# Performance work log

Measured on AMD Instinct MI355X. Metric: run time of the kernel, lower is better.

## Reference

```python
import jax, jax.numpy as jnp
import numpy as np

B, T, D = 32, 512, 768
K, H = 256, 512


def setup_inputs() -> dict:
    key = jax.random.key(0)
    ks = jax.random.split(key, 5)
    s = 0.02  # keep pre-activations in a sane range
    return {
        "inputs": jax.random.normal(ks[0], (B, T, D), jnp.float32),
        "W_x": jax.random.normal(ks[1], (K + 1, 4 * H), jnp.float32) * s,
        "W_h": jax.random.normal(ks[2], (H, 4 * H), jnp.float32) * s,
        "b_lstm": jnp.zeros((4 * H,), jnp.float32),
        "W_key": jax.random.normal(ks[3], (H, K), jnp.float32) * s,
        "b_key": jnp.zeros((K,), jnp.float32),
        "W_g": jax.random.normal(ks[4], (H, 1), jnp.float32) * s,
        "b_g": jnp.zeros((1,), jnp.float32),
        "conf_gain": jnp.ones((), jnp.float32),
        "conf_bias": jnp.zeros((), jnp.float32),
    }


def reference(inputs, W_x, W_h, b_lstm, W_key, b_key, W_g, b_g, conf_gain, conf_bias):
    Bq, Tq, Dq = inputs.shape
    Kq = W_key.shape[1]
    Hq = W_h.shape[0]
    t_idx = jnp.arange(Tq)
    xs = jnp.transpose(inputs, (1, 0, 2))  # [T, B, D]

    def step(carry, xt):
        t, x = xt  # t: scalar step index, x: [B, D]
        key_r, h, c, M_k, M_v = carry
        # Keras LSTMCell (gate order i, f, c, o); input is previous key_r [B, K+1]
        z = key_r @ W_x + h @ W_h + b_lstm
        i, f, g_c, o = jnp.split(z, 4, axis=-1)
        i = jax.nn.sigmoid(i)
        f = jax.nn.sigmoid(f)
        g_c = jnp.tanh(g_c)
        o = jax.nn.sigmoid(o)
        c = f * c + i * g_c
        h = o * jnp.tanh(c)  # lstm_out == hidden in Keras LSTMCell
        key_w = h @ W_key + b_key            # [B, K]
        g = jax.nn.sigmoid(h @ W_g + b_g)    # [B, 1]
        # similarity attention over all previously written memory slots
        sim = jnp.einsum('bd,tbd->bt', x, M_v)          # [B, T]
        mask = (t_idx < t)[None, :]                     # valid slots only
        w_k = jax.nn.softmax(jnp.where(mask, sim, -1e30), axis=1)
        c_k = jax.nn.sigmoid(sim * conf_gain + conf_bias)
        aug = jnp.concatenate([jnp.transpose(M_k, (1, 0, 2)), c_k[:, :, None]], axis=2)  # [B, T, K+1]
        key_r_new = jnp.where(t > 0, g * jnp.einsum('bt,btk->bk', w_k, aug), 0.0)
        M_k = M_k.at[t].set(key_w)
        M_v = M_v.at[t].set(x)
        return (key_r_new, h, c, M_k, M_v), None

    init = (
        jnp.zeros((Bq, Kq + 1), inputs.dtype),
        jnp.zeros((Bq, Hq), inputs.dtype),
        jnp.zeros((Bq, Hq), inputs.dtype),
        jnp.zeros((Tq, Bq, Kq), inputs.dtype),
        jnp.zeros((Tq, Bq, Dq), inputs.dtype),
    )
    (key_r, h, c, M_k, M_v), _ = jax.lax.scan(step, init, (t_idx, xs))
    return h  # final lstm_out
```

## Files before the change

### kernel.cpp

```cpp
#include <hip/hip_runtime.h>
#include <math.h>

#define BQ 32
#define TQ 512
#define DQ 768
#define KQ 256
#define HQ 512
#define G4 2048
#define SROW 772
#define NWG 512
#define NTHR 256
#define NBG 4

typedef float f32x4 __attribute__((ext_vector_type(4)));

__device__ __forceinline__ void waitcnt0() {
  asm volatile("s_waitcnt vmcnt(0) lgkmcnt(0)" ::: "memory");
}
__device__ __forceinline__ void st_agent(float* p, float v) {
  asm volatile("global_store_dword %0, %1, off sc0 sc1" :: "v"(p), "v"(v) : "memory");
}
__device__ __forceinline__ int ld_flag(const int* p) {
  int v;
  asm volatile("global_load_dword %0, %1, off sc0 sc1\ns_waitcnt vmcnt(0)"
               : "=v"(v) : "v"(p) : "memory");
  return v;
}
__device__ __forceinline__ void wg_wait(const int* flags, int target) {
  const int lane = threadIdx.x & 63;
  for (;;) {
    int v = ld_flag(flags + lane);
    if (__all(v >= target)) break;
    __builtin_amdgcn_s_sleep(1);
  }
  __syncthreads();
}
__device__ __forceinline__ void wg_signal(int* flag, int val) {
  waitcnt0();
  __syncthreads();
  if (threadIdx.x == 0)
    asm volatile("global_store_dword %0, %1, off sc0 sc1" :: "v"(flag), "v"(val) : "memory");
}
__device__ __forceinline__ float sigm(float x) { return 1.f / (1.f + __expf(-x)); }

__global__ void __launch_bounds__(256) gram_k(const float* __restrict__ X,
                                              float* __restrict__ Gm) {
  __shared__ __align__(16) float As[64 * 33];
  __shared__ __align__(16) float Bs[64 * 33];
  const int bid = blockIdx.x;
  const int b = blockIdx.y;
  int I = 0, base = 0;
  while (base + I + 1 <= bid) { base += I + 1; ++I; }
  const int J = bid - base;
  const int t0 = I * 64, u0 = J * 64;
  const float* Xb = X + (size_t)b * TQ * DQ;
  const int ty = threadIdx.x >> 4, tx = threadIdx.x & 15;
  const int sc = threadIdx.x & 31, sr = threadIdx.x >> 5;
  float acc[4][4];
#pragma unroll
  for (int i = 0; i < 4; ++i)
#pragma unroll
    for (int j = 0; j < 4; ++j) acc[i][j] = 0.f;
  for (int k0 = 0; k0 < DQ; k0 += 32) {
#pragma unroll
    for (int rr = 0; rr < 8; ++rr) {
      const int r = rr * 8 + sr;
      As[r * 33 + sc] = Xb[(size_t)(t0 + r) * DQ + k0 + sc];
      Bs[r * 33 + sc] = Xb[(size_t)(u0 + r) * DQ + k0 + sc];
    }
    __syncthreads();
#pragma unroll
    for (int k = 0; k < 32; ++k) {
      float av[4], bv[4];
#pragma unroll
      for (int i = 0; i < 4; ++i) av[i] = As[(ty * 4 + i) * 33 + k];
#pragma unroll
      for (int j = 0; j < 4; ++j) bv[j] = Bs[(tx * 4 + j) * 33 + k];
#pragma unroll
      for (int i = 0; i < 4; ++i)
#pragma unroll
        for (int j = 0; j < 4; ++j) acc[i][j] += av[i] * bv[j];
    }
    __syncthreads();
  }
  float* gb = Gm + (size_t)b * TQ * TQ;
#pragma unroll
  for (int i = 0; i < 4; ++i) {
    f32x4 o;
    o.x = acc[i][0]; o.y = acc[i][1]; o.z = acc[i][2]; o.w = acc[i][3];
    *(f32x4*)&gb[(size_t)(t0 + ty * 4 + i) * TQ + u0 + tx * 4] = o;
  }
}

__global__ void __launch_bounds__(256) smax_k(float* __restrict__ Gm,
                                              float* __restrict__ Sv,
                                              const float* __restrict__ cgp,
                                              const float* __restrict__ cbp) {
  const int t = blockIdx.x + 1;
  const int b = blockIdx.y;
  const int tid = threadIdx.x;
  const int lane = tid & 63;
  const int wv = tid >> 6;
  __shared__ float row[TQ];
  __shared__ float r1[4], r2[4], r3[4];
  float* R = Gm + ((size_t)b * TQ + t) * TQ;
  const float cg = cgp[0], cb = cbp[0];
  for (int i = tid; i < t; i += 256) row[i] = R[i];
  __syncthreads();
  float m = -3e38f;
  for (int i = tid; i < t; i += 256) m = fmaxf(m, row[i]);
#pragma unroll
  for (int k = 1; k < 64; k <<= 1) m = fmaxf(m, __shfl_xor(m, k));
  if (lane == 0) r1[wv] = m;
  __syncthreads();
  m = fmaxf(fmaxf(r1[0], r1[1]), fmaxf(r1[2], r1[3]));
  float s = 0.f, sck = 0.f;
  for (int i = tid; i < t; i += 256) {
    const float r = row[i];
    const float e = __expf(r - m);
    const float ck = 1.f / (1.f + __expf(-(r * cg + cb)));
    row[i] = e; s += e; sck += e * ck;
  }
#pragma unroll
  for (int k = 1; k < 64; k <<= 1) { s += __shfl_xor(s, k); sck += __shfl_xor(sck, k); }
  if (lane == 0) { r2[wv] = s; r3[wv] = sck; }
  __syncthreads();
  s = r2[0] + r2[1] + r2[2] + r2[3];
  sck = r3[0] + r3[1] + r3[2] + r3[3];
  const float inv = 1.f / s;
  for (int i = tid; i < t; i += 256) R[i] = row[i] * inv;
  if (tid == 0) Sv[(size_t)b * TQ + t] = sck * inv;
}

__global__ void __launch_bounds__(NTHR, 2) esbn_scan(
    const float* __restrict__ Wx, const float* __restrict__ Wh,
    const float* __restrict__ bl, const float* __restrict__ Wk,
    const float* __restrict__ bk, const float* __restrict__ Wg,
    const float* __restrict__ bgp, const float* __restrict__ Wmat,
    const float* __restrict__ Sv, float* buf, int* flagsX, int* flagsY,
    float* __restrict__ out) {
  __shared__ __align__(16) float st[NBG * SROW];
  __shared__ __align__(16) float wrow[NBG * TQ];
  __shared__ __align__(16) float Mk_s[16 * 520];
  __shared__ __align__(16) float wkey_s[4 * 520];
  __shared__ float wgv[HQ];
  __shared__ __align__(16) float zred[4 * 8 * 4 * 4];
  __shared__ float c_s[NBG * 8];
  __shared__ float gg_s[NBG];
  __shared__ float A_s[NBG * 4];
  __shared__ float bl_s[32];
  __shared__ float bk_s[4];
  __shared__ float bg_s;

  const int tid = threadIdx.x;
  const int wg = blockIdx.x & 63;
  const int grp = blockIdx.x >> 6;
  const int b0 = grp * NBG;
  const int dc = tid >> 3;
  const int cg = tid & 7;

  int colg[4];
#pragma unroll
  for (int j = 0; j < 4; ++j) {
    const int c = cg * 4 + j;
    colg[j] = (c >> 3) * HQ + wg * 8 + (c & 7);
  }
  f32x4 wh[16], wxr[8], wxl;
#pragma unroll
  for (int i = 0; i < 16; ++i) {
    const int d = (i << 5) + dc;
    wh[i].x = Wh[(size_t)d * G4 + colg[0]];
    wh[i].y = Wh[(size_t)d * G4 + colg[1]];
    wh[i].z = Wh[(size_t)d * G4 + colg[2]];
    wh[i].w = Wh[(size_t)d * G4 + colg[3]];
  }
#pragma unroll
  for (int i = 0; i < 8; ++i) {
    const int d = (i << 5) + dc;
    wxr[i].x = Wx[(size_t)d * G4 + colg[0]];
    wxr[i].y = Wx[(size_t)d * G4 + colg[1]];
    wxr[i].z = Wx[(size_t)d * G4 + colg[2]];
    wxr[i].w = Wx[(size_t)d * G4 + colg[3]];
  }
  wxl.x = wxl.y = wxl.z = wxl.w = 0.f;
  if (dc == 0) {
    wxl.x = Wx[(size_t)256 * G4 + colg[0]];
    wxl.y = Wx[(size_t)256 * G4 + colg[1]];
    wxl.z = Wx[(size_t)256 * G4 + colg[2]];
    wxl.w = Wx[(size_t)256 * G4 + colg[3]];
  }
  for (int i = tid; i < NBG * SROW; i += NTHR) st[i] = 0.f;
  for (int i = tid; i < 16 * 520; i += NTHR) Mk_s[i] = 0.f;
  for (int i = tid; i < 4 * 520; i += NTHR) {
    const int kl = i / 520, u = i - kl * 520;
    wkey_s[i] = (u < HQ) ? Wk[(size_t)u * KQ + wg * 4 + kl] : 0.f;
  }
  for (int i = tid; i < HQ; i += NTHR) wgv[i] = Wg[i];
  if (tid < 32) bl_s[tid] = bl[(tid >> 3) * HQ + wg * 8 + (tid & 7)];
  if (tid < 4) bk_s[tid] = bk[wg * 4 + tid];
  if (tid == 0) bg_s = bgp[0];
  if (tid < NBG * 8) c_s[tid] = 0.f;
  if (tid < NBG * 4) A_s[tid] = 0.f;
  __syncthreads();

  int* fx = flagsX + grp * 64;
  int* fy = flagsY + grp * 64;
  const int yb = tid >> 6;
  const int ykl = (tid >> 4) & 3;
  const int ytc = tid & 15;
  const int lt = tid & 63;

  for (int t = 0; t < TQ; ++t) {
    const int p = t & 1, pn = p ^ 1;
    f32x4 acc[NBG];
#pragma unroll
    for (int b = 0; b < NBG; ++b) { acc[b].x = 0.f; acc[b].y = 0.f; acc[b].z = 0.f; acc[b].w = 0.f; }
#pragma unroll
    for (int i = 0; i < 16; ++i) {
      const f32x4 w = wh[i];
      const int d = (i << 5) + dc;
#pragma unroll
      for (int b = 0; b < NBG; ++b) acc[b] += st[b * SROW + d] * w;
    }
    wg_wait(fy, t);
    {
      float* base = buf + (size_t)(p * BQ + b0) * SROW;
      const int r0 = tid / 65, o0 = tid - r0 * 65;
      const float* q0 = base + r0 * SROW + 512 + (o0 << 2);
      f32x4 u0, u1;
      u1.x = u1.y = u1.z = u1.w = 0.f;
      asm volatile("global_load_dwordx4 %0, %1, off sc0 sc1" : "=v"(u0) : "v"(q0));
      if (tid < 4) {
        const int j1 = tid + 256;
        const int r1 = j1 / 65, o1 = j1 - r1 * 65;
        const float* q1 = base + r1 * SROW + 512 + (o1 << 2);
        asm volatile("global_load_dwordx4 %0, %1, off sc0 sc1" : "=v"(u1) : "v"(q1));
      }
      asm volatile("s_waitcnt vmcnt(0)" : "+v"(u0), "+v"(u1) : : "memory");
      *(f32x4*)&st[r0 * SROW + 512 + (o0 << 2)] = u0;
      if (tid < 4) {
        const int j1 = tid + 256;
        const int r1 = j1 / 65, o1 = j1 - r1 * 65;
        *(f32x4*)&st[r1 * SROW + 512 + (o1 << 2)] = u1;
      }
    }
    __syncthreads();
#pragma unroll
    for (int i = 0; i < 8; ++i) {
      const f32x4 w = wxr[i];
      const int d = 512 + (i << 5) + dc;
#pragma unroll
      for (int b = 0; b < NBG; ++b) acc[b] += st[b * SROW + d] * w;
    }
    if (dc == 0) {
#pragma unroll
      for (int b = 0; b < NBG; ++b) acc[b] += st[b * SROW + 768] * wxl;
    }
#pragma unroll
    for (int m = 8; m <= 32; m <<= 1) {
#pragma unroll
      for (int b = 0; b < NBG; ++b) {
        acc[b].x += __shfl_xor(acc[b].x, m);
        acc[b].y += __shfl_xor(acc[b].y, m);
        acc[b].z += __shfl_xor(acc[b].z, m);
        acc[b].w += __shfl_xor(acc[b].w, m);
      }
    }
    if (lt < 8) {
      const int wv = tid >> 6;
#pragma unroll
      for (int b = 0; b < NBG; ++b)
        *(f32x4*)&zred[((wv * 8 + lt) * 4 + b) * 4] = acc[b];
    }
    __syncthreads();
    if (tid < 32) {
      const int b = tid >> 3, u = tid & 7;
      float zg[4];
#pragma unroll
      for (int g = 0; g < 4; ++g) {
        const int cgi = g * 2 + (u >> 2), comp = u & 3;
        float z = bl_s[g * 8 + u];
#pragma unroll
        for (int wv = 0; wv < 4; ++wv) z += zred[((wv * 8 + cgi) * 4 + b) * 4 + comp];
        zg[g] = z;
      }
      const float gi = sigm(zg[0]);
      const float gf = sigm(zg[1]);
      const float go = sigm(zg[3]);
      const float cn = gf * c_s[tid] + gi * tanhf(zg[2]);
      const float hv = go * tanhf(cn);
      c_s[tid] = cn;
      st_agent(buf + (size_t)(pn * BQ + b0 + b) * SROW + wg * 8 + u, hv);
      if (t == TQ - 1) out[(size_t)(b0 + b) * HQ + wg * 8 + u] = hv;
    }
    wg_signal(&fx[wg], t + 1);
    if (t == TQ - 1) break;

    if (t > 0) {
      const float* wr = Wmat + ((size_t)(b0 + yb) * TQ + t) * TQ;
#pragma unroll
      for (int k = 0; k < 8; ++k) {
        const int u = lt + (k << 6);
        wrow[yb * TQ + u] = (u < t) ? wr[u] : 0.f;
      }
    }
    __syncthreads();
    float accA = 0.f;
    if (t > 0) {
      const float* mk = &Mk_s[(yb * 4 + ykl) * 520];
      const float* wb = &wrow[yb * TQ];
#pragma unroll
      for (int j = 0; j < 32; ++j) {
        const int u = ytc + (j << 4);
        accA += wb[u] * mk[u];
      }
      accA += __shfl_xor(accA, 1);
      accA += __shfl_xor(accA, 2);
      accA += __shfl_xor(accA, 4);
      accA += __shfl_xor(accA, 8);
    }
    if (ytc == 0) A_s[yb * 4 + ykl] = accA;
    wg_wait(fx, t + 1);
    {
      float* base = buf + (size_t)(pn * BQ + b0) * SROW;
      f32x4 v0, v1;
      const int i0 = tid, i1 = tid + 256;
      const float* p0 = base + (i0 >> 7) * SROW + ((i0 & 127) << 2);
      const float* p1v = base + (i1 >> 7) * SROW + ((i1 & 127) << 2);
      asm volatile("global_load_dwordx4 %0, %1, off sc0 sc1" : "=v"(v0) : "v"(p0));
      asm volatile("global_load_dwordx4 %0, %1, off sc0 sc1" : "=v"(v1) : "v"(p1v));
      asm volatile("s_waitcnt vmcnt(0)" : "+v"(v0), "+v"(v1) : : "memory");
      *(f32x4*)&st[(i0 >> 7) * SROW + ((i0 & 127) << 2)] = v0;
      *(f32x4*)&st[(i1 >> 7) * SROW + ((i1 & 127) << 2)] = v1;
    }
    __syncthreads();
    {
      float a = 0.f;
#pragma unroll
      for (int k = 0; k < 8; ++k) {
        const int u = lt + (k << 6);
        a += st[yb * SROW + u] * wgv[u];
      }
#pragma unroll
      for (int m = 1; m <= 32; m <<= 1) a += __shfl_xor(a, m);
      if (lt == 0) gg_s[yb] = sigm(a + bg_s);
    }
    __syncthreads();
    if (ytc == 0)
      st_agent(buf + (size_t)(pn * BQ + b0 + yb) * SROW + 512 + wg * 4 + ykl,
               gg_s[yb] * A_s[yb * 4 + ykl]);
    if (wg == 63 && lt == 0)
      st_agent(buf + (size_t)(pn * BQ + b0 + yb) * SROW + 512 + 256,
               gg_s[yb] * Sv[(size_t)(b0 + yb) * TQ + t]);
    wg_signal(&fy[wg], t + 1);
    {
      float kw = 0.f;
      const float* hrow = &st[yb * SROW];
      const float* wkr = &wkey_s[ykl * 520];
#pragma unroll
      for (int j = 0; j < 32; ++j) {
        const int u = ytc + (j << 4);
        kw += hrow[u] * wkr[u];
      }
      kw += __shfl_xor(kw, 1);
      kw += __shfl_xor(kw, 2);
      kw += __shfl_xor(kw, 4);
      kw += __shfl_xor(kw, 8);
      if (ytc == 0) Mk_s[(yb * 4 + ykl) * 520 + t] = kw + bk_s[ykl];
    }
  }
}

extern "C" void kernel_launch(void* const* d_in, const int* in_sizes, int n_in,
                              void* d_out, int out_size, void* d_ws, size_t ws_size,
                              hipStream_t stream) {
  (void)in_sizes; (void)n_in; (void)out_size; (void)ws_size;
  const float* X  = (const float*)d_in[0];
  const float* Wx = (const float*)d_in[1];
  const float* Wh = (const float*)d_in[2];
  const float* bl = (const float*)d_in[3];
  const float* Wk = (const float*)d_in[4];
  const float* bk = (const float*)d_in[5];
  const float* Wg = (const float*)d_in[6];
  const float* bg = (const float*)d_in[7];
  const float* cg = (const float*)d_in[8];
  const float* cb = (const float*)d_in[9];
  float* out = (float*)d_out;
  float* ws = (float*)d_ws;

  float* Gm = ws;
  float* Sv = ws + (size_t)8388608;
  float* buf = ws + (size_t)8404992;
  int* flagsX = (int*)(ws + (size_t)8454400);
  int* flagsY = flagsX + 512;

  hipMemsetAsync(Sv, 0, (size_t)(16384 + 49408 + 1024) * 4, stream);
  gram_k<<<dim3(36, BQ), dim3(256), 0, stream>>>(X, Gm);
  smax_k<<<dim3(TQ - 1, BQ), dim3(256), 0, stream>>>(Gm, Sv, cg, cb);

  void* args[] = {(void*)&Wx, (void*)&Wh, (void*)&bl, (void*)&Wk, (void*)&bk,
                  (void*)&Wg, (void*)&bg, (void*)&Gm, (void*)&Sv,
                  (void*)&buf, (void*)&flagsX, (void*)&flagsY, (void*)&out};
  hipError_t e = hipLaunchCooperativeKernel((const void*)esbn_scan, dim3(NWG),
                                            dim3(NTHR), args, 0, stream);
  if (e != hipSuccess) {
    esbn_scan<<<dim3(NWG), dim3(NTHR), 0, stream>>>(Wx, Wh, bl, Wk, bk, Wg, bg,
                                                    Gm, Sv, buf, flagsX,
                                                    flagsY, out);
  }
}
```

Baseline: 4.951 ms.

## Merge two per-step grid barriers into one by deferring gate scaling

Restructures the recurrent step so that each workgroup publishes its h slice and its unscaled attention readout together, then signals a single flag per step instead of two. The gate g is computed locally from h after the barrier and applied to the key_r contribution inside the z accumulation, rather than scaled before publication. The Wmat row loads are also prefetched early into registers. This removes one cross-workgroup barrier round trip per timestep, at the cost of each workgroup recomputing g and reading a larger combined buffer.

```diff
diff --git a/kernel.cpp b/kernel.cpp
--- a/kernel.cpp
+++ b/kernel.cpp
@@ -139,6 +139,7 @@
     const float* __restrict__ bgp, const float* __restrict__ Wmat,
     const float* __restrict__ Sv, float* buf, int* flagsX, int* flagsY,
     float* __restrict__ out) {
+  (void)flagsY;
   __shared__ __align__(16) float st[NBG * SROW];
   __shared__ __align__(16) float wrow[NBG * TQ];
   __shared__ __align__(16) float Mk_s[16 * 520];
@@ -147,7 +148,6 @@
   __shared__ __align__(16) float zred[4 * 8 * 4 * 4];
   __shared__ float c_s[NBG * 8];
   __shared__ float gg_s[NBG];
-  __shared__ float A_s[NBG * 4];
   __shared__ float bl_s[32];
   __shared__ float bk_s[4];
   __shared__ float bg_s;
@@ -200,21 +200,67 @@
   if (tid < 4) bk_s[tid] = bk[wg * 4 + tid];
   if (tid == 0) bg_s = bgp[0];
   if (tid < NBG * 8) c_s[tid] = 0.f;
-  if (tid < NBG * 4) A_s[tid] = 0.f;
-  __syncthreads();
-
-  int* fx = flagsX + grp * 64;
-  int* fy = flagsY + grp * 64;
+  __syncthreads();
+
+  int* f = flagsX + grp * 64;
   const int yb = tid >> 6;
   const int ykl = (tid >> 4) & 3;
   const int ytc = tid & 15;
   const int lt = tid & 63;
 
+  const int i0 = tid, i1 = tid + 256, i2 = tid + 512;
+  const int sb0 = i0 / 192, so0 = i0 - sb0 * 192;
+  const int sb1 = i1 / 192, so1 = i1 - sb1 * 192;
+  const int sb2 = i2 / 192, so2 = i2 - sb2 * 192;
+  const int sj0 = sb0 * SROW + ((so0 < 128) ? (so0 << 2) : (512 + ((so0 - 128) << 2)));
+  const int sj1 = sb1 * SROW + ((so1 < 128) ? (so1 << 2) : (512 + ((so1 - 128) << 2)));
+  const int sj2 = sb2 * SROW + ((so2 < 128) ? (so2 << 2) : (512 + ((so2 - 128) << 2)));
+
   for (int t = 0; t < TQ; ++t) {
     const int p = t & 1, pn = p ^ 1;
-    f32x4 acc[NBG];
-#pragma unroll
-    for (int b = 0; b < NBG; ++b) { acc[b].x = 0.f; acc[b].y = 0.f; acc[b].z = 0.f; acc[b].w = 0.f; }
+    float wv8[8];
+    const bool rowv = (t >= 1) && (t < TQ - 1);
+    if (rowv) {
+      const float* wr = Wmat + ((size_t)(b0 + yb) * TQ + t) * TQ + lt;
+#pragma unroll
+      for (int k = 0; k < 8; ++k) wv8[k] = wr[k << 6];
+    }
+    if (t > 0) {
+      wg_wait(f, t);
+      float* base = buf + (size_t)(p * BQ + b0) * SROW;
+      f32x4 v0, v1, v2;
+      const float* q0 = base + sj0;
+      const float* q1 = base + sj1;
+      const float* q2 = base + sj2;
+      asm volatile("global_load_dwordx4 %0, %1, off sc0 sc1" : "=v"(v0) : "v"(q0));
+      asm volatile("global_load_dwordx4 %0, %1, off sc0 sc1" : "=v"(v1) : "v"(q1));
+      asm volatile("global_load_dwordx4 %0, %1, off sc0 sc1" : "=v"(v2) : "v"(q2));
+      float sv = 0.f;
+      if (tid < 4) sv = Sv[(size_t)(b0 + tid) * TQ + (t - 1)];
+      asm volatile("s_waitcnt vmcnt(0)" : "+v"(v0), "+v"(v1), "+v"(v2) : : "memory");
+      *(f32x4*)&st[sj0] = v0;
+      *(f32x4*)&st[sj1] = v1;
+      *(f32x4*)&st[sj2] = v2;
+      if (tid < 4) st[tid * SROW + 768] = sv;
+    }
+    __syncthreads();
+    {
+      float a = 0.f;
+#pragma unroll
+      for (int k = 0; k < 8; ++k) {
+        const int u = lt + (k << 6);
+        a += st[yb * SROW + u] * wgv[u];
+      }
+#pragma unroll
+      for (int m = 1; m <= 32; m <<= 1) a += __shfl_xor(a, m);
+      if (lt == 0) gg_s[yb] = sigm(a + bg_s);
+    }
+    f32x4 acc[NBG], pk[NBG];
+#pragma unroll
+    for (int b = 0; b < NBG; ++b) {
+      acc[b].x = acc[b].y = acc[b].z = acc[b].w = 0.f;
+      pk[b].x = pk[b].y = pk[b].z = pk[b].w = 0.f;
+    }
 #pragma unroll
     for (int i = 0; i < 16; ++i) {
       const f32x4 w = wh[i];
@@ -222,39 +268,23 @@
 #pragma unroll
       for (int b = 0; b < NBG; ++b) acc[b] += st[b * SROW + d] * w;
     }
-    wg_wait(fy, t);
-    {
-      float* base = buf + (size_t)(p * BQ + b0) * SROW;
-      const int r0 = tid / 65, o0 = tid - r0 * 65;
-      const float* q0 = base + r0 * SROW + 512 + (o0 << 2);
-      f32x4 u0, u1;
-      u1.x = u1.y = u1.z = u1.w = 0.f;
-      asm volatile("global_load_dwordx4 %0, %1, off sc0 sc1" : "=v"(u0) : "v"(q0));
-      if (tid < 4) {
-        const int j1 = tid + 256;
-        const int r1 = j1 / 65, o1 = j1 - r1 * 65;
-        const float* q1 = base + r1 * SROW + 512 + (o1 << 2);
-        asm volatile("global_load_dwordx4 %0, %1, off sc0 sc1" : "=v"(u1) : "v"(q1));
-      }
-      asm volatile("s_waitcnt vmcnt(0)" : "+v"(u0), "+v"(u1) : : "memory");
-      *(f32x4*)&st[r0 * SROW + 512 + (o0 << 2)] = u0;
-      if (tid < 4) {
-        const int j1 = tid + 256;
-        const int r1 = j1 / 65, o1 = j1 - r1 * 65;
-        *(f32x4*)&st[r1 * SROW + 512 + (o1 << 2)] = u1;
-      }
-    }
-    __syncthreads();
 #pragma unroll
     for (int i = 0; i < 8; ++i) {
       const f32x4 w = wxr[i];
       const int d = 512 + (i << 5) + dc;
 #pragma unroll
-      for (int b = 0; b < NBG; ++b) acc[b] += st[b * SROW + d] * w;
+      for (int b = 0; b < NBG; ++b) pk[b] += st[b * SROW + d] * w;
     }
     if (dc == 0) {
 #pragma unroll
-      for (int b = 0; b < NBG; ++b) acc[b] += st[b * SROW + 768] * wxl;
+      for (int b = 0; b < NBG; ++b) pk[b] += st[b * SROW + 768] * wxl;
+    }
+    __syncthreads();
+#pragma unroll
+    for (int b = 0; b < NBG; ++b) {
+      const float g = gg_s[b];
+      acc[b].x += g * pk[b].x; acc[b].y += g * pk[b].y;
+      acc[b].z += g * pk[b].z; acc[b].w += g * pk[b].w;
     }
 #pragma unroll
     for (int m = 8; m <= 32; m <<= 1) {
@@ -290,23 +320,27 @@
       const float cn = gf * c_s[tid] + gi * tanhf(zg[2]);
       const float hv = go * tanhf(cn);
       c_s[tid] = cn;
-      st_agent(buf + (size_t)(pn * BQ + b0 + b) * SROW + wg * 8 + u, hv);
       if (t == TQ - 1) out[(size_t)(b0 + b) * HQ + wg * 8 + u] = hv;
-    }
-    wg_signal(&fx[wg], t + 1);
+      else st_agent(buf + (size_t)(pn * BQ + b0 + b) * SROW + wg * 8 + u, hv);
+    }
     if (t == TQ - 1) break;
-
-    if (t > 0) {
-      const float* wr = Wmat + ((size_t)(b0 + yb) * TQ + t) * TQ;
-#pragma unroll
-      for (int k = 0; k < 8; ++k) {
-        const int u = lt + (k << 6);
-        wrow[yb * TQ + u] = (u < t) ? wr[u] : 0.f;
-      }
-    }
-    __syncthreads();
-    float accA = 0.f;
-    if (t > 0) {
+    if (t >= 1) {
+#pragma unroll
+      for (int k = 0; k < 8; ++k) wrow[yb * TQ + lt + (k << 6)] = wv8[k];
+      float kw = 0.f;
+      const float* hrow = &st[yb * SROW];
+      const float* wkr = &wkey_s[ykl * 520];
+#pragma unroll
+      for (int j = 0; j < 32; ++j) {
+        const int u = ytc + (j << 4);
+        kw += hrow[u] * wkr[u];
+      }
+      kw += __shfl_xor(kw, 1);
+      kw += __shfl_xor(kw, 2);
+      kw += __shfl_xor(kw, 4);
+      kw += __shfl_xor(kw, 8);
+      if (ytc == 0) Mk_s[(yb * 4 + ykl) * 520 + (t - 1)] = kw + bk_s[ykl];
+      float accA = 0.f;
       const float* mk = &Mk_s[(yb * 4 + ykl) * 520];
       const float* wb = &wrow[yb * TQ];
 #pragma unroll
@@ -318,56 +352,10 @@
       accA += __shfl_xor(accA, 2);
       accA += __shfl_xor(accA, 4);
       accA += __shfl_xor(accA, 8);
-    }
-    if (ytc == 0) A_s[yb * 4 + ykl] = accA;
-    wg_wait(fx, t + 1);
-    {
-      float* base = buf + (size_t)(pn * BQ + b0) * SROW;
-      f32x4 v0, v1;
-      const int i0 = tid, i1 = tid + 256;
-      const float* p0 = base + (i0 >> 7) * SROW + ((i0 & 127) << 2);
-      const float* p1v = base + (i1 >> 7) * SROW + ((i1 & 127) << 2);
-      asm volatile("global_load_dwordx4 %0, %1, off sc0 sc1" : "=v"(v0) : "v"(p0));
-      asm volatile("global_load_dwordx4 %0, %1, off sc0 sc1" : "=v"(v1) : "v"(p1v));
-      asm volatile("s_waitcnt vmcnt(0)" : "+v"(v0), "+v"(v1) : : "memory");
-      *(f32x4*)&st[(i0 >> 7) * SROW + ((i0 & 127) << 2)] = v0;
-      *(f32x4*)&st[(i1 >> 7) * SROW + ((i1 & 127) << 2)] = v1;
-    }
-    __syncthreads();
-    {
-      float a = 0.f;
-#pragma unroll
-      for (int k = 0; k < 8; ++k) {
-        const int u = lt + (k << 6);
-        a += st[yb * SROW + u] * wgv[u];
-      }
-#pragma unroll
-      for (int m = 1; m <= 32; m <<= 1) a += __shfl_xor(a, m);
-      if (lt == 0) gg_s[yb] = sigm(a + bg_s);
-    }
-    __syncthreads();
-    if (ytc == 0)
-      st_agent(buf + (size_t)(pn * BQ + b0 + yb) * SROW + 512 + wg * 4 + ykl,
-               gg_s[yb] * A_s[yb * 4 + ykl]);
-    if (wg == 63 && lt == 0)
-      st_agent(buf + (size_t)(pn * BQ + b0 + yb) * SROW + 512 + 256,
-               gg_s[yb] * Sv[(size_t)(b0 + yb) * TQ + t]);
-    wg_signal(&fy[wg], t + 1);
-    {
-      float kw = 0.f;
-      const float* hrow = &st[yb * SROW];
-      const float* wkr = &wkey_s[ykl * 520];
-#pragma unroll
-      for (int j = 0; j < 32; ++j) {
-        const int u = ytc + (j << 4);
-        kw += hrow[u] * wkr[u];
-      }
-      kw += __shfl_xor(kw, 1);
-      kw += __shfl_xor(kw, 2);
-      kw += __shfl_xor(kw, 4);
-      kw += __shfl_xor(kw, 8);
-      if (ytc == 0) Mk_s[(yb * 4 + ykl) * 520 + t] = kw + bk_s[ykl];
-    }
+      if (ytc == 0)
+        st_agent(buf + (size_t)(pn * BQ + b0 + yb) * SROW + 512 + wg * 4 + ykl, accA);
+    }
+    wg_signal(&f[wg], t + 1);
   }
 }
 
```

Result: slower. 5.133 ms (+3.7%).
